# Optimization experiments

Measured on AMD Instinct MI355X. Metric: run time of the kernel, lower is better.

## Reference

```python
import jax, jax.numpy as jnp
import numpy as np

ATT_DIM = 2048
NUM_HEADS = 16
NUM_KV_GROUPS = 4
HEAD_DIM = 128
CONTEXT_LENGTH = 2048
ROPE_BASE = 10000.0
GROUP_SIZE = NUM_HEADS // NUM_KV_GROUPS
BATCH = 2


def _precompute_rope_sin(context_length, head_dim, rope_base):
    # thetas over rope_dim = head_dim // 2, exponent uses rope_dim (as in source)
    rope_dim = head_dim // 2
    j = jnp.arange(rope_dim, dtype=jnp.float32)
    thetas = 1.0 / rope_base ** (2.0 * j / rope_dim)
    positions = jnp.arange(context_length, dtype=jnp.float32)
    angles = positions[:, None] * thetas[None, :]          # [CD, HD//2]
    angles = jnp.concatenate([angles, angles], axis=-1)    # [CD, HD]
    return jnp.sin(angles)                                  # cos is unused (see bug note)


def _apply_rope(qk, sin):
    # FAITHFUL to source bug: in compute_rope, `cos` is overwritten with the
    # broadcast `sin`, so the returned value is qk*sin + qk_2*sin.
    hd = qk.shape[-1]
    qkr = qk[..., : hd // 2]
    qki = qk[..., hd // 2 :]
    qk2 = jnp.concatenate([-qki, qkr], axis=-1)
    sin_b = sin[None, None, : qk.shape[2], :]
    return qk * sin_b + qk2 * sin  # second term broadcasts full-length sin (requires cd==context_length)


def setup_inputs() -> dict:
    key = jax.random.key(0)
    ks = jax.random.split(key, 6)
    s = 0.02
    x = jax.random.normal(ks[0], (BATCH, CONTEXT_LENGTH, ATT_DIM), dtype=jnp.float32)
    Wq = jax.random.normal(ks[1], (ATT_DIM, HEAD_DIM * NUM_HEADS), dtype=jnp.float32) * s
    Wk = jax.random.normal(ks[2], (ATT_DIM, HEAD_DIM * NUM_KV_GROUPS), dtype=jnp.float32) * s
    Wv = jax.random.normal(ks[3], (ATT_DIM, HEAD_DIM * NUM_KV_GROUPS), dtype=jnp.float32) * s
    Wo = jax.random.normal(ks[4], (HEAD_DIM * NUM_HEADS, HEAD_DIM * NUM_HEADS), dtype=jnp.float32) * s
    bo = jax.random.normal(ks[5], (HEAD_DIM * NUM_HEADS,), dtype=jnp.float32) * s
    return {"x": x, "Wq": Wq, "Wk": Wk, "Wv": Wv, "Wo": Wo, "bo": bo}


def reference(x, Wq, Wk, Wv, Wo, bo):
    bd, cd, ed = x.shape
    sin = _precompute_rope_sin(CONTEXT_LENGTH, HEAD_DIM, ROPE_BASE)

    q = (x @ Wq).reshape(bd, cd, NUM_HEADS, HEAD_DIM).transpose(0, 2, 1, 3)      # [B,NH,CD,HD]
    k = (x @ Wk).reshape(bd, cd, NUM_KV_GROUPS, HEAD_DIM).transpose(0, 2, 1, 3)  # [B,Nkv,CD,HD]
    v = (x @ Wv).reshape(bd, cd, NUM_KV_GROUPS, HEAD_DIM).transpose(0, 2, 1, 3)

    q = _apply_rope(q, sin)
    k = _apply_rope(k, sin)

    k = jnp.repeat(k, GROUP_SIZE, axis=1)  # [B,NH,CD,HD]
    v = jnp.repeat(v, GROUP_SIZE, axis=1)

    a = jnp.einsum("bhqd,bhkd->bhqk", q, k)  # [B,NH,CD,CD]
    causal = jnp.triu(jnp.ones((cd, cd), dtype=bool), k=1)
    a = jnp.where(causal[None, None], -jnp.inf, a)
    a = jax.nn.softmax(a / jnp.sqrt(jnp.float32(HEAD_DIM)), axis=-1)

    y = jnp.einsum("bhqk,bhkd->bhqd", a, v)                # [B,NH,CD,HD]
    y = y.transpose(0, 2, 1, 3).reshape(bd, cd, HEAD_DIM * NUM_HEADS)
    return y @ Wo + bo
```

## Files before the change

### kernel.cpp

```cpp
#include <hip/hip_runtime.h>
#include <hip/hip_bf16.h>
#include <cstdint>
#include <cstddef>

#define BATCH 2
#define CTX 2048
#define EMB 2048
#define NH 16
#define NG 4
#define HD 128
#define NQK (EMB + 2*NG*HD)
#define MROWS (BATCH*CTX)

typedef __bf16 bf16x8 __attribute__((ext_vector_type(8)));
typedef float  f32x4  __attribute__((ext_vector_type(4)));
typedef float  f32x16 __attribute__((ext_vector_type(16)));

__device__ __forceinline__ ushort f2bf(float f) {
    uint32_t u = __float_as_uint(f);
    u += 0x7FFFu + ((u >> 16) & 1u);
    return (ushort)(u >> 16);
}

__device__ __forceinline__ float bf2f(ushort u) {
    return __uint_as_float((uint32_t)u << 16);
}

__device__ __forceinline__ uint32_t packbf(float a, float b) {
    ushort lo = __builtin_bit_cast(ushort, (__bf16)a);
    ushort hi = __builtin_bit_cast(ushort, (__bf16)b);
    return (uint32_t)lo | ((uint32_t)hi << 16);
}

__device__ __forceinline__ bf16x8 mkfrag(uint32_t a, uint32_t b, uint32_t c, uint32_t d) {
    union { uint32_t u[4]; bf16x8 v; } z;
    z.u[0] = a; z.u[1] = b; z.u[2] = c; z.u[3] = d;
    return z.v;
}

__device__ __forceinline__ void gload_lds16(const void* g, void* l) {
    __builtin_amdgcn_global_load_lds((const __attribute__((address_space(1))) void*)g,
                                     (__attribute__((address_space(3))) void*)l, 16, 0, 0);
}

#define PREP_SIN 512
#define PREP_CVT 4096
__global__ __launch_bounds__(256) void k_prep(const float* __restrict__ x,
                                              const float* __restrict__ Wq, const float* __restrict__ Wk,
                                              const float* __restrict__ Wv, const float* __restrict__ Wo,
                                              float* __restrict__ sintab, ushort* __restrict__ xb,
                                              ushort* __restrict__ Wt, ushort* __restrict__ Wot) {
    int B = blockIdx.x;
    int tid = threadIdx.x;
    if (B < PREP_SIN) {
        int t = B * 256 + tid;
        int j = t & 63, p = t >> 6;
        float theta = 1.0f / powf(10000.0f, (float)(2 * j) / 64.0f);
        sintab[t] = sinf((float)p * theta);
        return;
    }
    if (B < PREP_SIN + PREP_CVT) {
        int i = (B - PREP_SIN) * 256 + tid;
        const float4* src = (const float4*)x;
        ushort4* dst = (ushort4*)xb;
        #pragma unroll
        for (int k = 0; k < 2; ++k) {
            float4 v = src[i*2 + k];
            ushort4 o;
            o.x = f2bf(v.x); o.y = f2bf(v.y); o.z = f2bf(v.z); o.w = f2bf(v.w);
            dst[i*2 + k] = o;
        }
        return;
    }
    __shared__ float tile[32][33];
    int zz = B - (PREP_SIN + PREP_CVT);
    int z = zz >> 12;
    int rem = zz & 4095;
    int bxx = rem & 63, byy = rem >> 6;
    const float* src; ushort* dst; int src_ld, ncols;
    if (z == 0)      { src = Wq; dst = Wt;                               src_ld = EMB;   ncols = EMB; }
    else if (z == 1) { src = Wk; dst = Wt + (size_t)EMB * EMB;           src_ld = NG*HD; ncols = NG*HD; }
    else if (z == 2) { src = Wv; dst = Wt + (size_t)(EMB + NG*HD) * EMB; src_ld = NG*HD; ncols = NG*HD; }
    else             { src = Wo; dst = Wot;                              src_ld = EMB;   ncols = EMB; }
    int c0 = bxx * 32, r0 = byy * 32;
    if (c0 >= ncols) return;
    int tx = tid & 31, ty = tid >> 5;
    #pragma unroll
    for (int i = 0; i < 4; ++i)
        tile[ty + i*8][tx] = src[(size_t)(r0 + ty + i*8) * src_ld + c0 + tx];
    __syncthreads();
    #pragma unroll
    for (int i = 0; i < 4; ++i)
        dst[(size_t)(c0 + ty + i*8) * EMB + r0 + tx] = f2bf(tile[tx][ty + i*8]);
}

#define CLDS_STRIDE 130
__global__ __launch_bounds__(256) void k_gemm_qkv(const ushort* __restrict__ A, const ushort* __restrict__ Bt,
                                                  const float* __restrict__ sintab,
                                                  ushort* __restrict__ Qf, ushort* __restrict__ Kf,
                                                  ushort* __restrict__ Vf, float qscale) {
    __shared__ __align__(16) char smem[33792];
    int tid = threadIdx.x;
    int lane = tid & 63;
    int wave = tid >> 6;
    int wr = wave >> 1, wc = wave & 1;

    int nbx = gridDim.x;
    int id  = blockIdx.y * nbx + blockIdx.x;
    int cpx = (nbx * gridDim.y) >> 3;
    int sid = (id & 7) * cpx + (id >> 3);
    int bx = sid % nbx, by = sid / nbx;
    int m0 = by * 128, n0 = bx * 128;

    int lr = lane & 15, lg = lane >> 4;

    f32x4 acc[4][4] = {};

    int arow = lane >> 2;
    int kpart = (lane & 3) * 8;

    ushort* As = (ushort*)smem;
    ushort* Bs = (ushort*)(smem + 16384);

    int c0s = (wave*2 + 0) * 512, c1s = (wave*2 + 1) * 512;
    const ushort* ga0 = A  + (size_t)(m0 + (wave*2+0)*16 + arow) * EMB + kpart;
    const ushort* ga1 = A  + (size_t)(m0 + (wave*2+1)*16 + arow) * EMB + kpart;
    const ushort* gb0 = Bt + (size_t)(n0 + (wave*2+0)*16 + arow) * EMB + kpart;
    const ushort* gb1 = Bt + (size_t)(n0 + (wave*2+1)*16 + arow) * EMB + kpart;

    auto stage = [&](int koff, int bufoff) {
        gload_lds16(ga0 + koff, &As[bufoff + c0s]);
        gload_lds16(ga1 + koff, &As[bufoff + c1s]);
        gload_lds16(gb0 + koff, &Bs[bufoff + c0s]);
        gload_lds16(gb1 + koff, &Bs[bufoff + c1s]);
    };
    auto compute = [&](int bufoff) {
        bf16x8 af[4], bfr[4];
        #pragma unroll
        for (int mt = 0; mt < 4; ++mt)
            af[mt] = *(const bf16x8*)&As[bufoff + (wr*64 + mt*16 + lr) * 32 + lg * 8];
        #pragma unroll
        for (int nt = 0; nt < 4; ++nt)
            bfr[nt] = *(const bf16x8*)&Bs[bufoff + (wc*64 + nt*16 + lr) * 32 + lg * 8];
        #pragma unroll
        for (int mt = 0; mt < 4; ++mt)
            #pragma unroll
            for (int nt = 0; nt < 4; ++nt)
                acc[mt][nt] = __builtin_amdgcn_mfma_f32_16x16x32_bf16(af[mt], bfr[nt], acc[mt][nt], 0, 0, 0);
    };

    const int nsteps = EMB / 32;
    stage(0, 0);
    __syncthreads();
    for (int t = 0; t + 2 < nsteps; t += 2) {
        stage(32, 4096);
        compute(0);
        __syncthreads();
        stage(64, 0);
        compute(4096);
        __syncthreads();
        ga0 += 64; ga1 += 64; gb0 += 64; gb1 += 64;
    }
    stage(32, 4096);
    compute(0);
    __syncthreads();
    compute(4096);
    __syncthreads();

    ushort* clds = (ushort*)smem;
    #pragma unroll
    for (int mt = 0; mt < 4; ++mt) {
        #pragma unroll
        for (int nt = 0; nt < 4; ++nt) {
            int col = wc*64 + nt*16 + lr;
            int row = wr*64 + mt*16 + lg*4;
            ushort2 p01, p23;
            p01.x = f2bf(acc[mt][nt][0]); p01.y = f2bf(acc[mt][nt][1]);
            p23.x = f2bf(acc[mt][nt][2]); p23.y = f2bf(acc[mt][nt][3]);
            *(ushort2*)&clds[col*CLDS_STRIDE + row]     = p01;
            *(ushort2*)&clds[col*CLDS_STRIDE + row + 2] = p23;
        }
    }
    __syncthreads();

    int xt = bx;
    int b = m0 >> 11;
    int pos0 = m0 & 2047;

    if (xt < 20) {
        int j = tid & 63;
        int rgrp = tid >> 6;
        ushort* dstb;
        float scl;
        if (xt < 16) { dstb = Qf + (size_t)((b*NH + xt) * 64) * 4096;      scl = qscale; }
        else         { dstb = Kf + (size_t)((b*NG + (xt-16)) * 64) * 4096; scl = 1.0f;   }
        #pragma unroll 4
        for (int it = 0; it < 32; ++it) {
            int row = rgrp + it*4;
            int pos = pos0 + row;
            float a  = bf2f(clds[j*CLDS_STRIDE + row]);
            float bb = bf2f(clds[(j+64)*CLDS_STRIDE + row]);
            float sv = sintab[pos*64 + j] * scl;
            size_t idx = (size_t)(pos>>5)*4096 + (size_t)(j>>4)*512 + ((j>>3)&1)*256 + (pos&31)*8 + (j&7);
            dstb[idx]        = f2bf((a - bb) * sv);
            dstb[idx + 2048] = f2bf((bb + a) * sv);
        }
    } else {
        int g = xt - 20;
        int bg = b*NG + g;
        int ln2 = tid & 31, hi2 = (tid >> 5) & 1, dt = tid >> 6;
        int colc = dt*32 + ln2;
        #pragma unroll
        for (int stp = 0; stp < 4; ++stp) {
            #pragma unroll
            for (int ks = 0; ks < 2; ++ks) {
                int rowb = stp*32 + ks*16 + hi2*8;
                union { ushort2 q[4]; bf16x8 v; } z;
                z.q[0] = *(ushort2*)&clds[colc*CLDS_STRIDE + rowb];
                z.q[1] = *(ushort2*)&clds[colc*CLDS_STRIDE + rowb + 2];
                z.q[2] = *(ushort2*)&clds[colc*CLDS_STRIDE + rowb + 4];
                z.q[3] = *(ushort2*)&clds[colc*CLDS_STRIDE + rowb + 6];
                int step_g = (pos0 >> 5) + stp;
                *(bf16x8*)(Vf + ((size_t)(bg*64 + step_g)*8 + dt*2 + ks) * 512 + (tid & 63) * 8) = z.v;
            }
        }
    }
}

__global__ __launch_bounds__(256) void k_gemm_bt(const ushort* __restrict__ A, const ushort* __restrict__ Bt,
                                                 float* __restrict__ C, int M, int N, int K,
                                                 const float* __restrict__ bias) {
    __shared__ __align__(16) ushort As[2][128 * 32];
    __shared__ __align__(16) ushort Bs[2][128 * 32];
    int tid = threadIdx.x;
    int lane = tid & 63;
    int wave = tid >> 6;
    int wr = wave >> 1, wc = wave & 1;

    int nbx = gridDim.x;
    int id  = blockIdx.y * nbx + blockIdx.x;
    int cpx = (nbx * gridDim.y) >> 3;
    int sid = (id & 7) * cpx + (id >> 3);
    int bx = sid % nbx, by = sid / nbx;
    int m0 = by * 128, n0 = bx * 128;

    int lr = lane & 15, lg = lane >> 4;

    f32x4 acc[4][4] = {};

    int arow = lane >> 2;
    int kpart = (lane & 3) * 8;

    int c0s = (wave*2 + 0) * 512, c1s = (wave*2 + 1) * 512;
    const ushort* ga0 = A  + (size_t)(m0 + (wave*2+0)*16 + arow) * K + kpart;
    const ushort* ga1 = A  + (size_t)(m0 + (wave*2+1)*16 + arow) * K + kpart;
    const ushort* gb0 = Bt + (size_t)(n0 + (wave*2+0)*16 + arow) * K + kpart;
    const ushort* gb1 = Bt + (size_t)(n0 + (wave*2+1)*16 + arow) * K + kpart;

    auto stage = [&](int koff, int buf) {
        gload_lds16(ga0 + koff, &As[buf][c0s]);
        gload_lds16(ga1 + koff, &As[buf][c1s]);
        gload_lds16(gb0 + koff, &Bs[buf][c0s]);
        gload_lds16(gb1 + koff, &Bs[buf][c1s]);
    };
    auto compute = [&](int buf) {
        bf16x8 af[4], bfr[4];
        #pragma unroll
        for (int mt = 0; mt < 4; ++mt)
            af[mt] = *(const bf16x8*)&As[buf][(wr*64 + mt*16 + lr) * 32 + lg * 8];
        #pragma unroll
        for (int nt = 0; nt < 4; ++nt)
            bfr[nt] = *(const bf16x8*)&Bs[buf][(wc*64 + nt*16 + lr) * 32 + lg * 8];
        #pragma unroll
        for (int mt = 0; mt < 4; ++mt)
            #pragma unroll
            for (int nt = 0; nt < 4; ++nt)
                acc[mt][nt] = __builtin_amdgcn_mfma_f32_16x16x32_bf16(af[mt], bfr[nt], acc[mt][nt], 0, 0, 0);
    };

    int nsteps = K >> 5;
    stage(0, 0);
    __syncthreads();
    for (int t = 0; t + 2 < nsteps; t += 2) {
        stage(32, 1);
        compute(0);
        __syncthreads();
        stage(64, 0);
        compute(1);
        __syncthreads();
        ga0 += 64; ga1 += 64; gb0 += 64; gb1 += 64;
    }
    stage(32, 1);
    compute(0);
    __syncthreads();
    compute(1);

    #pragma unroll
    for (int mt = 0; mt < 4; ++mt) {
        #pragma unroll
        for (int nt = 0; nt < 4; ++nt) {
            int col = n0 + wc*64 + nt*16 + lr;
            float bv = bias ? bias[col] : 0.0f;
            #pragma unroll
            for (int r = 0; r < 4; ++r) {
                int row = m0 + wr*64 + mt*16 + lg*4 + r;
                C[(size_t)row * N + col] = acc[mt][nt][r] + bv;
            }
        }
    }
}

__global__ __launch_bounds__(512) void k_attn14(const ushort* __restrict__ Qf, const ushort* __restrict__ Kf,
                                                const ushort* __restrict__ Vf, ushort* __restrict__ y) {
    __shared__ __align__(16) char smem[66048];
    int tid  = threadIdx.x;
    int lane = tid & 63;
    int w    = tid >> 6;
    int hh   = w >> 1, ww = w & 1;
    int B  = blockIdx.x;
    int bg = B & 7;
    int t  = 63 - (B >> 3);
    int b = bg >> 2, g = bg & 3, h = g * 4 + hh;
    int ln = lane & 31, hi = lane >> 5;
    int q0 = t * 32;

    const ushort* kf_g = Kf + (size_t)bg * 64 * 4096;
    const ushort* vf_g = Vf + (size_t)bg * 64 * 4096;

    auto stageKV = [&](int r) {
        #pragma unroll
        for (int s2 = 0; s2 < 2; ++s2) {
            gload_lds16(kf_g + r*8192 + s2*4096 + tid*8, smem + 32768 + s2*8192 + tid*16);
            gload_lds16(vf_g + r*8192 + s2*4096 + tid*8, smem + 49152 + s2*8192 + tid*16);
        }
    };

    #pragma unroll
    for (int s = 0; s < 4; ++s) {
        const ushort* qsrc = Qf + ((size_t)((b*NH + g*4 + s) * 64 + t)) * 4096 + tid * 8;
        gload_lds16(qsrc, smem + s*8192 + tid*16);
    }
    stageKV(0);
    __syncthreads();

    const char* qsl = smem + hh*8192  + lane*16;
    const char* ksl = smem + 32768 + ww*8192 + lane*16;
    const char* vsl = smem + 49152 + ww*8192 + lane*16;

    f32x16 od[4] = {};
    float lsum = 0.0f;

    auto step = [&](bool diag) {
        f32x16 st = {};
        #pragma unroll
        for (int s = 0; s < 8; ++s) {
            bf16x8 kf = *(const bf16x8*)(ksl + s * 1024);
            bf16x8 qf = *(const bf16x8*)(qsl + s * 1024);
            st = __builtin_amdgcn_mfma_f32_32x32x16_bf16(kf, qf, st, 0, 0, 0);
        }
        if (diag) {
            #pragma unroll
            for (int r = 0; r < 16; ++r) {
                int kl = (r & 3) + 8*(r >> 2) + 4*hi;
                if (kl > ln) st[r] = -1e30f;
            }
        }
        #pragma unroll
        for (int r = 0; r < 16; ++r) st[r] = exp2f(st[r]);
        float s8[8];
        #pragma unroll
        for (int r = 0; r < 8; ++r) s8[r] = st[r] + st[r+8];
        #pragma unroll
        for (int r = 0; r < 4; ++r) s8[r] = s8[r] + s8[r+4];
        lsum += (s8[0] + s8[1]) + (s8[2] + s8[3]);

        #pragma unroll
        for (int ks = 0; ks < 2; ++ks) {
            uint32_t w0 = packbf(st[8*ks+0], st[8*ks+1]);
            uint32_t w1 = packbf(st[8*ks+2], st[8*ks+3]);
            uint32_t w2 = packbf(st[8*ks+4], st[8*ks+5]);
            uint32_t w3 = packbf(st[8*ks+6], st[8*ks+7]);
            uint32_t sa = hi ? w0 : w2;
            uint32_t sb = hi ? w1 : w3;
            uint32_t ra = (uint32_t)__shfl_xor((int)sa, 32, 64);
            uint32_t rb = (uint32_t)__shfl_xor((int)sb, 32, 64);
            bf16x8 pa = hi ? mkfrag(ra, rb, w2, w3) : mkfrag(w0, w1, ra, rb);
            #pragma unroll
            for (int dt = 0; dt < 4; ++dt) {
                bf16x8 vf = *(const bf16x8*)(vsl + (dt*2 + ks) * 1024);
                od[dt] = __builtin_amdgcn_mfma_f32_32x32x16_bf16(pa, vf, od[dt], 0, 0, 0);
            }
        }
    };

    int rounds = (t >> 1) + 1;
    for (int r = 0; r < rounds; ++r) {
        int tile = 2*r + ww;
        if (tile <= t) step(tile == t);
        __syncthreads();
        if (r + 1 < rounds) {
            stageKV(r + 1);
            __syncthreads();
        }
    }

    lsum += __shfl_xor(lsum, 32, 64);

    float* sOd = (float*)(smem + hh*16512);
    float* sl  = (float*)(smem + hh*16512 + 16384);
    if (ww == 1) {
        #pragma unroll
        for (int r = 0; r < 16; ++r) {
            int ri = (r & 3) + 8*(r >> 2) + 4*hi;
            #pragma unroll
            for (int dt = 0; dt < 4; ++dt) sOd[ri*128 + dt*32 + ln] = od[dt][r];
        }
        if (hi == 0) sl[ln] = lsum;
    }
    __syncthreads();
    if (ww == 0) {
        float inv = 1.0f / (lsum + sl[ln]);
        #pragma unroll
        for (int r = 0; r < 16; ++r) {
            int ri = (r & 3) + 8*(r >> 2) + 4*hi;
            float ivr = __shfl(inv, ri, 64);
            int row = q0 + ri;
            #pragma unroll
            for (int dt = 0; dt < 4; ++dt) {
                float v = (od[dt][r] + sOd[ri*128 + dt*32 + ln]) * ivr;
                y[((size_t)(b*CTX + row)) * (NH*HD) + h*HD + dt*32 + ln] = f2bf(v);
            }
        }
    }
}

#define SIN_OFF   ((size_t)0)
#define XB_OFF    ((size_t)524288)
#define WT_OFF    ((size_t)17301504)
#define WOT_OFF   ((size_t)29884416)
#define QB_OFF    ((size_t)88604672)
#define KB_OFF    ((size_t)105381888)
#define VT_OFF    ((size_t)109576192)
#define YB_OFF    ((size_t)113770496)

extern "C" void kernel_launch(void* const* d_in, const int* in_sizes, int n_in,
                              void* d_out, int out_size, void* d_ws, size_t ws_size,
                              hipStream_t stream) {
    const float* x  = (const float*)d_in[0];
    const float* Wq = (const float*)d_in[1];
    const float* Wk = (const float*)d_in[2];
    const float* Wv = (const float*)d_in[3];
    const float* Wo = (const float*)d_in[4];
    const float* bo = (const float*)d_in[5];
    float* out = (float*)d_out;
    char* ws = (char*)d_ws;

    float*  sintab = (float*)(ws + SIN_OFF);
    ushort* xb     = (ushort*)(ws + XB_OFF);
    ushort* Wt     = (ushort*)(ws + WT_OFF);
    ushort* Wot    = (ushort*)(ws + WOT_OFF);
    ushort* Qf     = (ushort*)(ws + QB_OFF);
    ushort* Kf     = (ushort*)(ws + KB_OFF);
    ushort* Vf     = (ushort*)(ws + VT_OFF);
    ushort* yb     = (ushort*)(ws + YB_OFF);

    const float qscale = 0.08838834764831845f * 1.4426950408889634f;

    k_prep<<<PREP_SIN + PREP_CVT + 4*4096, 256, 0, stream>>>(x, Wq, Wk, Wv, Wo, sintab, xb, Wt, Wot);
    k_gemm_qkv<<<dim3(NQK/128, MROWS/128), 256, 0, stream>>>(xb, Wt, sintab, Qf, Kf, Vf, qscale);
    k_attn14<<<512, 512, 0, stream>>>(Qf, Kf, Vf, yb);
    k_gemm_bt<<<dim3(EMB/128, MROWS/128), 256, 0, stream>>>(yb, Wot, out, MROWS, EMB, EMB, bo);
}
```

Measured before the change: 199.8 us.

## Keep Q in registers and double-buffer K/V tiles in attention

Q fragments for each wave are now loaded once from global memory into registers instead of being staged through shared memory. The freed shared memory holds a second K/V buffer, so the next tile's async loads are issued before the current tile is computed. This removes one barrier per round and hides load latency behind the MFMA work. The cost is more register pressure from the eight Q fragments, and the pipeline depends on the end-of-round barrier also waiting for the async LDS loads.

```diff
diff --git a/kernel.cpp b/kernel.cpp
--- a/kernel.cpp
+++ b/kernel.cpp
@@ -310,9 +310,10 @@
     }
 }
 
-__global__ __launch_bounds__(512) void k_attn14(const ushort* __restrict__ Qf, const ushort* __restrict__ Kf,
+__global__ __launch_bounds__(512) void k_attn15(const ushort* __restrict__ Qf, const ushort* __restrict__ Kf,
                                                 const ushort* __restrict__ Vf, ushort* __restrict__ y) {
     __shared__ __align__(16) char smem[66048];
+
     int tid  = threadIdx.x;
     int lane = tid & 63;
     int w    = tid >> 6;
@@ -327,36 +328,35 @@
     const ushort* kf_g = Kf + (size_t)bg * 64 * 4096;
     const ushort* vf_g = Vf + (size_t)bg * 64 * 4096;
 
-    auto stageKV = [&](int r) {
+    auto stageKV = [&](int r, int bufoff) {
         #pragma unroll
         for (int s2 = 0; s2 < 2; ++s2) {
-            gload_lds16(kf_g + r*8192 + s2*4096 + tid*8, smem + 32768 + s2*8192 + tid*16);
-            gload_lds16(vf_g + r*8192 + s2*4096 + tid*8, smem + 49152 + s2*8192 + tid*16);
-        }
-    };
-
-    #pragma unroll
-    for (int s = 0; s < 4; ++s) {
-        const ushort* qsrc = Qf + ((size_t)((b*NH + g*4 + s) * 64 + t)) * 4096 + tid * 8;
-        gload_lds16(qsrc, smem + s*8192 + tid*16);
-    }
-    stageKV(0);
-    __syncthreads();
-
-    const char* qsl = smem + hh*8192  + lane*16;
-    const char* ksl = smem + 32768 + ww*8192 + lane*16;
-    const char* vsl = smem + 49152 + ww*8192 + lane*16;
+            gload_lds16(kf_g + r*8192 + s2*4096 + tid*8, smem + bufoff + s2*8192 + tid*16);
+            gload_lds16(vf_g + r*8192 + s2*4096 + tid*8, smem + bufoff + 16384 + s2*8192 + tid*16);
+        }
+    };
+
+    bf16x8 qf[8];
+    {
+        const ushort* qsrc = Qf + ((size_t)((b*NH + h) * 64 + t)) * 4096 + lane * 8;
+        #pragma unroll
+        for (int s = 0; s < 8; ++s) qf[s] = *(const bf16x8*)(qsrc + s * 512);
+    }
+
+    stageKV(0, 0);
+    __syncthreads();
 
     f32x16 od[4] = {};
     float lsum = 0.0f;
 
-    auto step = [&](bool diag) {
+    auto step = [&](int bufoff, bool diag) {
+        const char* ksl = smem + bufoff + ww*8192 + lane*16;
+        const char* vsl = smem + bufoff + 16384 + ww*8192 + lane*16;
         f32x16 st = {};
         #pragma unroll
         for (int s = 0; s < 8; ++s) {
             bf16x8 kf = *(const bf16x8*)(ksl + s * 1024);
-            bf16x8 qf = *(const bf16x8*)(qsl + s * 1024);
-            st = __builtin_amdgcn_mfma_f32_32x32x16_bf16(kf, qf, st, 0, 0, 0);
+            st = __builtin_amdgcn_mfma_f32_32x32x16_bf16(kf, qf[s], st, 0, 0, 0);
         }
         if (diag) {
             #pragma unroll
@@ -395,13 +395,10 @@
 
     int rounds = (t >> 1) + 1;
     for (int r = 0; r < rounds; ++r) {
+        if (r + 1 < rounds) stageKV(r + 1, ((r + 1) & 1) ? 32768 : 0);
         int tile = 2*r + ww;
-        if (tile <= t) step(tile == t);
+        if (tile <= t) step((r & 1) ? 32768 : 0, tile == t);
         __syncthreads();
-        if (r + 1 < rounds) {
-            stageKV(r + 1);
-            __syncthreads();
-        }
     }
 
     lsum += __shfl_xor(lsum, 32, 64);
@@ -468,6 +465,6 @@
 
     k_prep<<<PREP_SIN + PREP_CVT + 4*4096, 256, 0, stream>>>(x, Wq, Wk, Wv, Wo, sintab, xb, Wt, Wot);
     k_gemm_qkv<<<dim3(NQK/128, MROWS/128), 256, 0, stream>>>(xb, Wt, sintab, Qf, Kf, Vf, qscale);
-    k_attn14<<<512, 512, 0, stream>>>(Qf, Kf, Vf, yb);
+    k_attn15<<<512, 512, 0, stream>>>(Qf, Kf, Vf, yb);
     k_gemm_bt<<<dim3(EMB/128, MROWS/128), 256, 0, stream>>>(yb, Wot, out, MROWS, EMB, EMB, bo);
 }
```

Result: faster. 190.4 us (median of 2 runs) (-4.7%).
